# Kernel tuning notes

Hardware: AMD Instinct MI355X
Metric: run time of the kernel (lower is better)

## Reference

```python
import jax, jax.numpy as jnp
import numpy as np

EMBED_DIM = 512
NUM_HEADS = 8
HEAD_DIM = EMBED_DIM // NUM_HEADS  # 64


def setup_inputs() -> dict:
    key = jax.random.key(0)
    ks = jax.random.split(key, 7)
    B, S, E = 4, 2048, EMBED_DIM
    std = 1.0 / np.sqrt(E)
    return {
        "x": jax.random.normal(ks[0], (B, S, E), dtype=jnp.float32),
        "wq": jax.random.uniform(ks[1], (E, E), jnp.float32, -std, std),
        "bq": jax.random.uniform(ks[2], (E,), jnp.float32, -std, std),
        "wk": jax.random.uniform(ks[3], (E, E), jnp.float32, -std, std),
        "bk": jax.random.uniform(ks[4], (E,), jnp.float32, -std, std),
        "wv": jax.random.uniform(ks[5], (E, E), jnp.float32, -std, std),
        "bv": jax.random.uniform(ks[6], (E,), jnp.float32, -std, std),
    }


def reference(x, wq, bq, wk, bk, wv, bv):
    B, S, E = x.shape
    H, D = NUM_HEADS, HEAD_DIM
    scaling = D ** (-0.5)

    def split_heads(t):  # [B,S,E] -> [B,H,S,D]
        return t.reshape(B, S, H, D).transpose(0, 2, 1, 3)

    q = split_heads(x @ wq + bq)
    k = split_heads(x @ wk + bk)
    v = split_heads(x @ wv + bv)

    # NOTE: original torch code DIVIDES by scaling (== multiply by sqrt(D)).
    scores = jnp.einsum("bhqd,bhkd->bhqk", q, k) / scaling
    weights = jax.nn.softmax(scores, axis=-1)
    ctx = jnp.einsum("bhqk,bhkd->bhqd", weights, v)  # [B,H,S,D]
    return ctx.transpose(0, 2, 1, 3).reshape(B, S, E)
```

## Files before the change

kernel.cpp:

```cpp
#include <hip/hip_runtime.h>
#include <hip/hip_bf16.h>


#define SE 2048
#define EB 512
#define BB 4
#define HH 8
#define DD 64
#define BHN (BB*HH)

typedef __attribute__((ext_vector_type(8))) short short8;
typedef __attribute__((ext_vector_type(4))) float f32x4;

#define MFMA16(a, b, c) __builtin_amdgcn_mfma_f32_16x16x32_bf16((a), (b), (c), 0, 0, 0)

#if __has_builtin(__builtin_amdgcn_exp2f)
#define EXP2(x) __builtin_amdgcn_exp2f(x)
#else
#define EXP2(x) exp2f(x)
#endif

__device__ __forceinline__ unsigned short f2bf(float f) {
    union { float f; unsigned u; } x; x.f = f;
    unsigned r = x.u + 0x7fffu + ((x.u >> 16) & 1u);
    return (unsigned short)(r >> 16);
}
__device__ __forceinline__ float bf2f(unsigned short b) {
    union { unsigned u; float f; } x; x.u = ((unsigned)b) << 16;
    return x.f;
}
__device__ __forceinline__ unsigned packbf2(float a, float b) {
    unsigned short lo = __bfloat16_as_ushort(__float2bfloat16(a));
    unsigned short hi = __bfloat16_as_ushort(__float2bfloat16(b));
    return (unsigned)lo | ((unsigned)hi << 16);
}

__global__ void xsplit_kernel(const float* __restrict__ x,
                              unsigned short* __restrict__ xh,
                              unsigned short* __restrict__ xl, int n4) {
    int i = blockIdx.x * blockDim.x + threadIdx.x;
    if (i >= n4) return;
    float4 v = reinterpret_cast<const float4*>(x)[i];
    float f[4] = {v.x, v.y, v.z, v.w};
    ushort4 hv, lv;
    unsigned short hh[4], ll[4];
#pragma unroll
    for (int j = 0; j < 4; j++) {
        hh[j] = f2bf(f[j]);
        ll[j] = f2bf(f[j] - bf2f(hh[j]));
    }
    hv.x = hh[0]; hv.y = hh[1]; hv.z = hh[2]; hv.w = hh[3];
    lv.x = ll[0]; lv.y = ll[1]; lv.z = ll[2]; lv.w = ll[3];
    reinterpret_cast<ushort4*>(xh)[i] = hv;
    reinterpret_cast<ushort4*>(xl)[i] = lv;
}

__global__ void wsplit_kernel(const float* __restrict__ wq, const float* __restrict__ wk,
                              const float* __restrict__ wv,
                              unsigned short* __restrict__ wth,
                              unsigned short* __restrict__ wtl) {
    int tid = blockIdx.x * blockDim.x + threadIdx.x;
    if (tid >= 3 * 512 * 512) return;
    int n = tid & 511;
    int k = (tid >> 9) & 511;
    int m = tid >> 18;
    const float* w = (m == 0) ? wq : ((m == 1) ? wk : wv);
    float v = w[k * 512 + n];
    unsigned short hb = f2bf(v);
    int o = ((m * 512 + n) << 9) + k;
    wth[o] = hb;
    wtl[o] = f2bf(v - bf2f(hb));
}

__device__ __forceinline__ void stage4(const unsigned short* __restrict__ g,
                                       char* lbase, int wave, int srow, int scol,
                                       int kk) {
#pragma unroll
    for (int j = 0; j < 4; j++) {
        __builtin_amdgcn_global_load_lds(
            (const __attribute__((address_space(1))) void*)(g + (size_t)(srow + j * 8) * 512 + kk + scol),
            (__attribute__((address_space(3))) void*)(lbase + wave * 4096 + j * 1024),
            16, 0, 0);
    }
}

template <int THREE>
__global__ __launch_bounds__(256) void proj_kernel(
    const unsigned short* __restrict__ xh, const unsigned short* __restrict__ xl,
    const unsigned short* __restrict__ wth, const unsigned short* __restrict__ wtl,
    const float* __restrict__ bq, const float* __restrict__ bk, const float* __restrict__ bv,
    unsigned short* __restrict__ qh, unsigned short* __restrict__ ql,
    unsigned short* __restrict__ kh, unsigned short* __restrict__ kl,
    unsigned short* __restrict__ vt) {
    constexpr int NTILE = THREE ? 4 : 2;
    __shared__ unsigned short lds[NTILE * 8192];
    char* LB = (char*)lds;
    constexpr int AHB = 0;
    constexpr int ALB = THREE ? 16384 : 0;
    constexpr int BHB = THREE ? 32768 : 16384;
    constexpr int BLB = THREE ? 49152 : 0;

    const int lane = threadIdx.x & 63;
    const int wave = threadIdx.x >> 6;
    const int lr = lane & 15, lk = lane >> 4;
    const int mat = THREE ? blockIdx.z : 2;
    const int m0 = blockIdx.x * 128;
    const int n0 = blockIdx.y * 128;
    const int wr = wave >> 1, wc = wave & 1;

    const unsigned short* Ah = xh + (size_t)m0 * 512;
    const unsigned short* Al = xl + (size_t)m0 * 512;
    const unsigned short* Bh = wth + (size_t)(mat * 512 + n0) * 512;
    const unsigned short* Bl = wtl + (size_t)(mat * 512 + n0) * 512;

    const int srow = wave * 32 + (lane >> 3);
    const int scol = 8 * ((lane & 7) ^ (lane >> 3));
    const int swzr = (lr & 7) << 4;

    f32x4 acc[4][4];
#pragma unroll
    for (int mi = 0; mi < 4; mi++)
#pragma unroll
        for (int ni = 0; ni < 4; ni++)
#pragma unroll
            for (int r = 0; r < 4; r++) acc[mi][ni][r] = 0.f;

    for (int t = 0; t < 8; t++) {
        const int kk = t * 64;
        stage4(Ah, LB + AHB, wave, srow, scol, kk);
        if (THREE) stage4(Al, LB + ALB, wave, srow, scol, kk);
        stage4(Bh, LB + BHB, wave, srow, scol, kk);
        if (THREE) stage4(Bl, LB + BLB, wave, srow, scol, kk);
        __syncthreads();

#pragma unroll
        for (int ks = 0; ks < 2; ks++) {
            short8 ah[4], al[4], bh8[4], bl8[4];
            const int cb = (ks * 64 + lk * 16) ^ swzr;
#pragma unroll
            for (int i = 0; i < 4; i++) {
                const int ao = (wr * 64 + i * 16 + lr) * 128 + cb;
                const int bo = (wc * 64 + i * 16 + lr) * 128 + cb;
                ah[i] = *reinterpret_cast<const short8*>(LB + AHB + ao);
                if (THREE) al[i] = *reinterpret_cast<const short8*>(LB + ALB + ao);
                bh8[i] = *reinterpret_cast<const short8*>(LB + BHB + bo);
                if (THREE) bl8[i] = *reinterpret_cast<const short8*>(LB + BLB + bo);
            }
#pragma unroll
            for (int mi = 0; mi < 4; mi++)
#pragma unroll
                for (int ni = 0; ni < 4; ni++) {
                    acc[mi][ni] = MFMA16(ah[mi], bh8[ni], acc[mi][ni]);
                    if (THREE) {
                        acc[mi][ni] = MFMA16(ah[mi], bl8[ni], acc[mi][ni]);
                        acc[mi][ni] = MFMA16(al[mi], bh8[ni], acc[mi][ni]);
                    }
                }
        }
        __syncthreads();
    }

    const float* bias = THREE ? ((mat == 0) ? bq : bk) : bv;
#pragma unroll
    for (int ni = 0; ni < 4; ni++) {
        const int col = n0 + wc * 64 + ni * 16 + lr;
        const float bsv = bias[col];
        const int h = col >> 6, d = col & 63;
#pragma unroll
        for (int mi = 0; mi < 4; mi++) {
#pragma unroll
            for (int r = 0; r < 4; r++) {
                const int row = m0 + wr * 64 + mi * 16 + lk * 4 + r;
                const int b_ = row >> 11, s = row & 2047;
                const int bh_ = b_ * HH + h;
                const float val = acc[mi][ni][r] + bsv;
                if (THREE) {
                    const unsigned short hb = f2bf(val);
                    const int o = (bh_ * SE + s) * DD + d;
                    if (mat == 0) { qh[o] = hb; ql[o] = f2bf(val - bf2f(hb)); }
                    else          { kh[o] = hb; kl[o] = f2bf(val - bf2f(hb)); }
                } else {
                    vt[(bh_ * DD + d) * SE + s] = f2bf(val);
                }
            }
        }
    }
}

__global__ __launch_bounds__(512, 4) void attn_kernel(
    const unsigned short* __restrict__ qh, const unsigned short* __restrict__ ql,
    const unsigned short* __restrict__ kh, const unsigned short* __restrict__ kl,
    const unsigned short* __restrict__ vt, float* __restrict__ out) {
    __shared__ char LB[65536];
    const int lane = threadIdx.x & 63, wave = threadIdx.x >> 6;
    const int lr = lane & 15, lk = lane >> 4;
    const int bh = blockIdx.x;
    const int b_ = bh >> 3, h = bh & 7;
    const int q0 = blockIdx.y * 128 + wave * 16;
    const int base = bh * SE * DD;
    const unsigned short* vbase = vt + bh * DD * SE;
    const float CL = 11.54156031f;
    const int swz = (lr & 7) << 4;

    const unsigned short* gp[3];
    int ginc[3], goff[3];
    {
        const int rIn = lane >> 3;
        const int c16 = (lane & 7) ^ rIn;
#pragma unroll
        for (int i = 0; i < 3; i++) {
            const int c = wave * 3 + i;
            const int mat = c >> 3, grp = c & 7;
            const int row = grp * 8 + rIn;
            if (mat == 0)      { gp[i] = kh + base + row * DD + c16 * 8;  ginc[i] = 64 * DD; }
            else if (mat == 1) { gp[i] = kl + base + row * DD + c16 * 8;  ginc[i] = 64 * DD; }
            else               { gp[i] = vbase + row * SE + c16 * 8;      ginc[i] = 64; }
            goff[i] = mat * 8192 + grp * 1024;
        }
    }

    short8 qhf[2], qlf[2];
    {
        const int qoff = base + (q0 + lr) * DD + lk * 8;
        qhf[0] = *reinterpret_cast<const short8*>(qh + qoff);
        qhf[1] = *reinterpret_cast<const short8*>(qh + qoff + 32);
        qlf[0] = *reinterpret_cast<const short8*>(ql + qoff);
        qlf[1] = *reinterpret_cast<const short8*>(ql + qoff + 32);
    }

    float m = -3.0e4f, l = 0.f;
    f32x4 o[4];
#pragma unroll
    for (int dnt = 0; dnt < 4; dnt++)
#pragma unroll
        for (int r = 0; r < 4; r++) o[dnt][r] = 0.f;

    char* myp = LB + 49152 + wave * 2048;

#pragma unroll
    for (int i = 0; i < 3; i++) {
        __builtin_amdgcn_global_load_lds(
            (const __attribute__((address_space(1))) void*)gp[i],
            (__attribute__((address_space(3))) void*)(LB + goff[i]), 16, 0, 0);
        gp[i] += ginc[i];
    }
    __syncthreads();

    for (int kt = 0; kt < 32; kt++) {
        const char* KB = LB + (kt & 1) * 24576;
        if (kt < 31) {
            const int nb = ((kt + 1) & 1) * 24576;
#pragma unroll
            for (int i = 0; i < 3; i++) {
                __builtin_amdgcn_global_load_lds(
                    (const __attribute__((address_space(1))) void*)gp[i],
                    (__attribute__((address_space(3))) void*)(LB + nb + goff[i]), 16, 0, 0);
                gp[i] += ginc[i];
            }
        }

        f32x4 s[4];
#pragma unroll
        for (int knt = 0; knt < 4; knt++)
#pragma unroll
            for (int r = 0; r < 4; r++) s[knt][r] = 0.f;

        __builtin_amdgcn_s_setprio(1);
#pragma unroll
        for (int knt = 0; knt < 4; knt++) {
            const int rb = (knt * 16 + lr) * 128;
            short8 kh0 = *reinterpret_cast<const short8*>(KB + rb + ((lk * 16) ^ swz));
            short8 kh1 = *reinterpret_cast<const short8*>(KB + rb + ((64 + lk * 16) ^ swz));
            short8 kl0 = *reinterpret_cast<const short8*>(KB + 8192 + rb + ((lk * 16) ^ swz));
            short8 kl1 = *reinterpret_cast<const short8*>(KB + 8192 + rb + ((64 + lk * 16) ^ swz));
            s[knt] = MFMA16(kh0, qhf[0], s[knt]);
            s[knt] = MFMA16(kh1, qhf[1], s[knt]);
            s[knt] = MFMA16(kl0, qhf[0], s[knt]);
            s[knt] = MFMA16(kl1, qhf[1], s[knt]);
            s[knt] = MFMA16(kh0, qlf[0], s[knt]);
            s[knt] = MFMA16(kh1, qlf[1], s[knt]);
        }
        __builtin_amdgcn_s_setprio(0);

        short8 vf[4][2];
#pragma unroll
        for (int dnt = 0; dnt < 4; dnt++) {
            const int rv = (dnt * 16 + lr) * 128;
            vf[dnt][0] = *reinterpret_cast<const short8*>(KB + 16384 + rv + ((lk * 16) ^ swz));
            vf[dnt][1] = *reinterpret_cast<const short8*>(KB + 16384 + rv + ((64 + lk * 16) ^ swz));
        }

        float mt = s[0][0];
#pragma unroll
        for (int knt = 0; knt < 4; knt++)
#pragma unroll
            for (int r = 0; r < 4; r++) mt = fmaxf(mt, s[knt][r]);
        mt = fmaxf(mt, __shfl_xor(mt, 16));
        mt = fmaxf(mt, __shfl_xor(mt, 32));

        if (!__all(mt <= m + 0.69314718f)) {
            const float mn = fmaxf(m, mt);
            const float fac = EXP2((m - mn) * CL);
            l *= fac;
#pragma unroll
            for (int dnt = 0; dnt < 4; dnt++)
#pragma unroll
                for (int r = 0; r < 4; r++) o[dnt][r] *= fac;
            m = mn;
        }
        const float nm = -m * CL;
        float rs = 0.f;
#pragma unroll
        for (int knt = 0; knt < 4; knt++) {
            float p0 = EXP2(fmaf(s[knt][0], CL, nm));
            float p1 = EXP2(fmaf(s[knt][1], CL, nm));
            float p2 = EXP2(fmaf(s[knt][2], CL, nm));
            float p3 = EXP2(fmaf(s[knt][3], CL, nm));
            rs += (p0 + p1) + (p2 + p3);
            unsigned w0 = packbf2(p0, p1);
            unsigned w1 = packbf2(p2, p3);
            const int cb = (knt * 32 + lk * 8) ^ swz;
            *reinterpret_cast<uint2*>(myp + lr * 128 + cb) = make_uint2(w0, w1);
        }
        rs += __shfl_xor(rs, 16);
        rs += __shfl_xor(rs, 32);
        l += rs;

        short8 pa0 = *reinterpret_cast<const short8*>(myp + lr * 128 + ((lk * 16) ^ swz));
        short8 pa1 = *reinterpret_cast<const short8*>(myp + lr * 128 + ((64 + lk * 16) ^ swz));
        __builtin_amdgcn_s_setprio(1);
#pragma unroll
        for (int dnt = 0; dnt < 4; dnt++) {
            o[dnt] = MFMA16(vf[dnt][0], pa0, o[dnt]);
            o[dnt] = MFMA16(vf[dnt][1], pa1, o[dnt]);
        }
        __builtin_amdgcn_s_setprio(0);

        __syncthreads();
    }

    const float rl = 1.0f / l;
    float* op = out + (size_t)(b_ * SE + q0 + lr) * EB + h * DD + lk * 4;
#pragma unroll
    for (int dnt = 0; dnt < 4; dnt++) {
        float4 val;
        val.x = o[dnt][0] * rl;
        val.y = o[dnt][1] * rl;
        val.z = o[dnt][2] * rl;
        val.w = o[dnt][3] * rl;
        *reinterpret_cast<float4*>(op + dnt * 16) = val;
    }
}

extern "C" void kernel_launch(void* const* d_in, const int* in_sizes, int n_in,
                              void* d_out, int out_size, void* d_ws, size_t ws_size,
                              hipStream_t stream) {
    const float* x  = (const float*)d_in[0];
    const float* wq = (const float*)d_in[1];
    const float* bq = (const float*)d_in[2];
    const float* wk = (const float*)d_in[3];
    const float* bk = (const float*)d_in[4];
    const float* wv = (const float*)d_in[5];
    const float* bv = (const float*)d_in[6];
    float* out = (float*)d_out;

    unsigned short* ws = (unsigned short*)d_ws;
    const int NX = 8192 * 512;
    const int NW = 3 * 512 * 512;
    const int NQ = BHN * SE * DD;
    unsigned short* xh  = ws;
    unsigned short* xl  = xh + NX;
    unsigned short* wth = xl + NX;
    unsigned short* wtl = wth + NW;
    unsigned short* qhp = wtl + NW;
    unsigned short* qlp = qhp + NQ;
    unsigned short* khp = qlp + NQ;
    unsigned short* klp = khp + NQ;
    unsigned short* vtp = klp + NQ;

    xsplit_kernel<<<NX / 4 / 256, 256, 0, stream>>>(x, xh, xl, NX / 4);
    wsplit_kernel<<<NW / 256, 256, 0, stream>>>(wq, wk, wv, wth, wtl);
    proj_kernel<1><<<dim3(64, 4, 2), 256, 0, stream>>>(xh, xl, wth, wtl, bq, bk, bv,
                                                       qhp, qlp, khp, klp, vtp);
    proj_kernel<0><<<dim3(64, 4), 256, 0, stream>>>(xh, xl, wth, wtl, bq, bk, bv,
                                                    qhp, qlp, khp, klp, vtp);
    attn_kernel<<<dim3(32, 16), 512, 0, stream>>>(qhp, qlp, khp, klp, vtp, out);
}
```

Measured before the change: 145.0 us.

## Switch attention to 32x32 MFMA tiles with register-shuffled P operand

```diff
diff --git a/kernel.cpp b/kernel.cpp
--- a/kernel.cpp
+++ b/kernel.cpp
@@ -11,8 +11,10 @@
 
 typedef __attribute__((ext_vector_type(8))) short short8;
 typedef __attribute__((ext_vector_type(4))) float f32x4;
+typedef __attribute__((ext_vector_type(16))) float f32x16;
 
 #define MFMA16(a, b, c) __builtin_amdgcn_mfma_f32_16x16x32_bf16((a), (b), (c), 0, 0, 0)
+#define MFMA32(a, b, c) __builtin_amdgcn_mfma_f32_32x32x16_bf16((a), (b), (c), 0, 0, 0)
 
 #if __has_builtin(__builtin_amdgcn_exp2f)
 #define EXP2(x) __builtin_amdgcn_exp2f(x)
@@ -187,29 +189,29 @@
     }
 }
 
-__global__ __launch_bounds__(512, 4) void attn_kernel(
+__global__ __launch_bounds__(256, 2) void attn_kernel(
     const unsigned short* __restrict__ qh, const unsigned short* __restrict__ ql,
     const unsigned short* __restrict__ kh, const unsigned short* __restrict__ kl,
     const unsigned short* __restrict__ vt, float* __restrict__ out) {
-    __shared__ char LB[65536];
+    __shared__ char LB[49152];
     const int lane = threadIdx.x & 63, wave = threadIdx.x >> 6;
-    const int lr = lane & 15, lk = lane >> 4;
+    const int q31 = lane & 31, hi = lane >> 5;
     const int bh = blockIdx.x;
     const int b_ = bh >> 3, h = bh & 7;
-    const int q0 = blockIdx.y * 128 + wave * 16;
+    const int q0 = blockIdx.y * 128 + wave * 32;
     const int base = bh * SE * DD;
     const unsigned short* vbase = vt + bh * DD * SE;
     const float CL = 11.54156031f;
-    const int swz = (lr & 7) << 4;
-
-    const unsigned short* gp[3];
-    int ginc[3], goff[3];
+    const int swz = (lane & 7) << 4;
+
+    const unsigned short* gp[6];
+    int ginc[6], goff[6];
     {
         const int rIn = lane >> 3;
         const int c16 = (lane & 7) ^ rIn;
 #pragma unroll
-        for (int i = 0; i < 3; i++) {
-            const int c = wave * 3 + i;
+        for (int i = 0; i < 6; i++) {
+            const int c = wave * 6 + i;
             const int mat = c >> 3, grp = c & 7;
             const int row = grp * 8 + rIn;
             if (mat == 0)      { gp[i] = kh + base + row * DD + c16 * 8;  ginc[i] = 64 * DD; }
@@ -219,26 +221,26 @@
         }
     }
 
-    short8 qhf[2], qlf[2];
+    short8 qhf[4], qlf[4];
     {
-        const int qoff = base + (q0 + lr) * DD + lk * 8;
-        qhf[0] = *reinterpret_cast<const short8*>(qh + qoff);
-        qhf[1] = *reinterpret_cast<const short8*>(qh + qoff + 32);
-        qlf[0] = *reinterpret_cast<const short8*>(ql + qoff);
-        qlf[1] = *reinterpret_cast<const short8*>(ql + qoff + 32);
+        const unsigned short* qb  = qh + base + (q0 + q31) * DD + 8 * hi;
+        const unsigned short* qlb = ql + base + (q0 + q31) * DD + 8 * hi;
+#pragma unroll
+        for (int ds = 0; ds < 4; ds++) {
+            qhf[ds] = *reinterpret_cast<const short8*>(qb + ds * 16);
+            qlf[ds] = *reinterpret_cast<const short8*>(qlb + ds * 16);
+        }
     }
 
     float m = -3.0e4f, l = 0.f;
-    f32x4 o[4];
-#pragma unroll
-    for (int dnt = 0; dnt < 4; dnt++)
-#pragma unroll
-        for (int r = 0; r < 4; r++) o[dnt][r] = 0.f;
-
-    char* myp = LB + 49152 + wave * 2048;
-
-#pragma unroll
-    for (int i = 0; i < 3; i++) {
+    f32x16 o[2];
+#pragma unroll
+    for (int dt = 0; dt < 2; dt++)
+#pragma unroll
+        for (int r = 0; r < 16; r++) o[dt][r] = 0.f;
+
+#pragma unroll
+    for (int i = 0; i < 6; i++) {
         __builtin_amdgcn_global_load_lds(
             (const __attribute__((address_space(1))) void*)gp[i],
             (__attribute__((address_space(3))) void*)(LB + goff[i]), 16, 0, 0);
@@ -251,7 +253,7 @@
         if (kt < 31) {
             const int nb = ((kt + 1) & 1) * 24576;
 #pragma unroll
-            for (int i = 0; i < 3; i++) {
+            for (int i = 0; i < 6; i++) {
                 __builtin_amdgcn_global_load_lds(
                     (const __attribute__((address_space(1))) void*)gp[i],
                     (__attribute__((address_space(3))) void*)(LB + nb + goff[i]), 16, 0, 0);
@@ -259,43 +261,45 @@
             }
         }
 
-        f32x4 s[4];
-#pragma unroll
-        for (int knt = 0; knt < 4; knt++)
-#pragma unroll
-            for (int r = 0; r < 4; r++) s[knt][r] = 0.f;
+        f32x16 s[2];
+#pragma unroll
+        for (int kt2 = 0; kt2 < 2; kt2++)
+#pragma unroll
+            for (int r = 0; r < 16; r++) s[kt2][r] = 0.f;
 
         __builtin_amdgcn_s_setprio(1);
 #pragma unroll
-        for (int knt = 0; knt < 4; knt++) {
-            const int rb = (knt * 16 + lr) * 128;
-            short8 kh0 = *reinterpret_cast<const short8*>(KB + rb + ((lk * 16) ^ swz));
-            short8 kh1 = *reinterpret_cast<const short8*>(KB + rb + ((64 + lk * 16) ^ swz));
-            short8 kl0 = *reinterpret_cast<const short8*>(KB + 8192 + rb + ((lk * 16) ^ swz));
-            short8 kl1 = *reinterpret_cast<const short8*>(KB + 8192 + rb + ((64 + lk * 16) ^ swz));
-            s[knt] = MFMA16(kh0, qhf[0], s[knt]);
-            s[knt] = MFMA16(kh1, qhf[1], s[knt]);
-            s[knt] = MFMA16(kl0, qhf[0], s[knt]);
-            s[knt] = MFMA16(kl1, qhf[1], s[knt]);
-            s[knt] = MFMA16(kh0, qlf[0], s[knt]);
-            s[knt] = MFMA16(kh1, qlf[1], s[knt]);
+        for (int kt2 = 0; kt2 < 2; kt2++) {
+            const int rb = (kt2 * 32 + q31) * 128;
+#pragma unroll
+            for (int ds = 0; ds < 4; ds++) {
+                const int cb = (ds * 32 + 16 * hi) ^ swz;
+                short8 khf = *reinterpret_cast<const short8*>(KB + rb + cb);
+                short8 klf = *reinterpret_cast<const short8*>(KB + 8192 + rb + cb);
+                s[kt2] = MFMA32(khf, qhf[ds], s[kt2]);
+                s[kt2] = MFMA32(khf, qlf[ds], s[kt2]);
+                s[kt2] = MFMA32(klf, qhf[ds], s[kt2]);
+            }
         }
         __builtin_amdgcn_s_setprio(0);
 
-        short8 vf[4][2];
-#pragma unroll
-        for (int dnt = 0; dnt < 4; dnt++) {
-            const int rv = (dnt * 16 + lr) * 128;
-            vf[dnt][0] = *reinterpret_cast<const short8*>(KB + 16384 + rv + ((lk * 16) ^ swz));
-            vf[dnt][1] = *reinterpret_cast<const short8*>(KB + 16384 + rv + ((64 + lk * 16) ^ swz));
+        short8 vf[2][2][2];
+#pragma unroll
+        for (int dt = 0; dt < 2; dt++) {
+            const int rv = (dt * 32 + q31) * 128;
+#pragma unroll
+            for (int kt2 = 0; kt2 < 2; kt2++)
+#pragma unroll
+                for (int f = 0; f < 2; f++)
+                    vf[dt][kt2][f] = *reinterpret_cast<const short8*>(
+                        KB + 16384 + rv + ((kt2 * 64 + f * 32 + 16 * hi) ^ swz));
         }
 
         float mt = s[0][0];
 #pragma unroll
-        for (int knt = 0; knt < 4; knt++)
-#pragma unroll
-            for (int r = 0; r < 4; r++) mt = fmaxf(mt, s[knt][r]);
-        mt = fmaxf(mt, __shfl_xor(mt, 16));
+        for (int kt2 = 0; kt2 < 2; kt2++)
+#pragma unroll
+            for (int r = 0; r < 16; r++) mt = fmaxf(mt, s[kt2][r]);
         mt = fmaxf(mt, __shfl_xor(mt, 32));
 
         if (!__all(mt <= m + 0.69314718f)) {
@@ -303,52 +307,62 @@
             const float fac = EXP2((m - mn) * CL);
             l *= fac;
 #pragma unroll
-            for (int dnt = 0; dnt < 4; dnt++)
-#pragma unroll
-                for (int r = 0; r < 4; r++) o[dnt][r] *= fac;
+            for (int dt = 0; dt < 2; dt++)
+#pragma unroll
+                for (int r = 0; r < 16; r++) o[dt][r] *= fac;
             m = mn;
         }
         const float nm = -m * CL;
         float rs = 0.f;
-#pragma unroll
-        for (int knt = 0; knt < 4; knt++) {
-            float p0 = EXP2(fmaf(s[knt][0], CL, nm));
-            float p1 = EXP2(fmaf(s[knt][1], CL, nm));
-            float p2 = EXP2(fmaf(s[knt][2], CL, nm));
-            float p3 = EXP2(fmaf(s[knt][3], CL, nm));
-            rs += (p0 + p1) + (p2 + p3);
-            unsigned w0 = packbf2(p0, p1);
-            unsigned w1 = packbf2(p2, p3);
-            const int cb = (knt * 32 + lk * 8) ^ swz;
-            *reinterpret_cast<uint2*>(myp + lr * 128 + cb) = make_uint2(w0, w1);
-        }
-        rs += __shfl_xor(rs, 16);
+
+#pragma unroll
+        for (int kt2 = 0; kt2 < 2; kt2++) {
+            float p[16];
+#pragma unroll
+            for (int r = 0; r < 16; r++) {
+                p[r] = EXP2(fmaf(s[kt2][r], CL, nm));
+                rs += p[r];
+            }
+            unsigned w[8];
+#pragma unroll
+            for (int j = 0; j < 8; j++) w[j] = packbf2(p[2 * j], p[2 * j + 1]);
+
+#pragma unroll
+            for (int f = 0; f < 2; f++) {
+                unsigned x0 = hi ? w[4 * f] : w[4 * f + 2];
+                unsigned x1 = hi ? w[4 * f + 1] : w[4 * f + 3];
+                unsigned y0 = __shfl_xor(x0, 32);
+                unsigned y1 = __shfl_xor(x1, 32);
+                union { unsigned u[4]; short8 s8; } pu;
+                pu.u[0] = hi ? y0 : w[4 * f];
+                pu.u[1] = hi ? y1 : w[4 * f + 1];
+                pu.u[2] = hi ? w[4 * f + 2] : y0;
+                pu.u[3] = hi ? w[4 * f + 3] : y1;
+                __builtin_amdgcn_s_setprio(1);
+                o[0] = MFMA32(vf[0][kt2][f], pu.s8, o[0]);
+                o[1] = MFMA32(vf[1][kt2][f], pu.s8, o[1]);
+                __builtin_amdgcn_s_setprio(0);
+            }
+        }
         rs += __shfl_xor(rs, 32);
         l += rs;
 
-        short8 pa0 = *reinterpret_cast<const short8*>(myp + lr * 128 + ((lk * 16) ^ swz));
-        short8 pa1 = *reinterpret_cast<const short8*>(myp + lr * 128 + ((64 + lk * 16) ^ swz));
-        __builtin_amdgcn_s_setprio(1);
-#pragma unroll
-        for (int dnt = 0; dnt < 4; dnt++) {
-            o[dnt] = MFMA16(vf[dnt][0], pa0, o[dnt]);
-            o[dnt] = MFMA16(vf[dnt][1], pa1, o[dnt]);
-        }
-        __builtin_amdgcn_s_setprio(0);
-
         __syncthreads();
     }
 
     const float rl = 1.0f / l;
-    float* op = out + (size_t)(b_ * SE + q0 + lr) * EB + h * DD + lk * 4;
-#pragma unroll
-    for (int dnt = 0; dnt < 4; dnt++) {
-        float4 val;
-        val.x = o[dnt][0] * rl;
-        val.y = o[dnt][1] * rl;
-        val.z = o[dnt][2] * rl;
-        val.w = o[dnt][3] * rl;
-        *reinterpret_cast<float4*>(op + dnt * 16) = val;
+    float* op = out + (size_t)(b_ * SE + q0 + q31) * EB + h * DD + 4 * hi;
+#pragma unroll
+    for (int dt = 0; dt < 2; dt++) {
+#pragma unroll
+        for (int a = 0; a < 4; a++) {
+            float4 val;
+            val.x = o[dt][4 * a + 0] * rl;
+            val.y = o[dt][4 * a + 1] * rl;
+            val.z = o[dt][4 * a + 2] * rl;
+            val.w = o[dt][4 * a + 3] * rl;
+            *reinterpret_cast<float4*>(op + dt * 32 + a * 8) = val;
+        }
     }
 }
 
@@ -384,5 +398,5 @@
                                                        qhp, qlp, khp, klp, vtp);
     proj_kernel<0><<<dim3(64, 4), 256, 0, stream>>>(xh, xl, wth, wtl, bq, bk, bv,
                                                     qhp, qlp, khp, klp, vtp);
-    attn_kernel<<<dim3(32, 16), 512, 0, stream>>>(qhp, qlp, khp, klp, vtp, out);
-}
+    attn_kernel<<<dim3(32, 16), 256, 0, stream>>>(qhp, qlp, khp, klp, vtp, out);
+}
```

After: 150.7 us. 3.9% more time.
